# Performance work log

Measured on AMD Instinct MI355X. Metric: run time of the kernel, lower is better.

## Reference

```python
import jax, jax.numpy as jnp
import numpy as np

B, S, D, H = 4, 1024, 1024, 16
DH = D // H  # head_dim = 64


def setup_inputs() -> dict:
    key = jax.random.key(0)
    kq, kk, kv, kl, kwq, kwk, kwv, kwo = jax.random.split(key, 8)
    query = jax.random.normal(kq, (B, S, D), dtype=jnp.float32)
    key_t = jax.random.normal(kk, (B, S, D), dtype=jnp.float32)
    value = jax.random.normal(kv, (B, S, D), dtype=jnp.float32)
    # padding: keys at positions >= valid length are padded (True)
    lengths = jax.random.randint(kl, (B,), S // 2, S + 1)
    key_padding_mask = jnp.arange(S)[None, :] >= lengths[:, None]  # [B,S] bool
    scale = 1.0 / np.sqrt(D)
    Wq = jax.random.normal(kwq, (D, D), dtype=jnp.float32) * scale
    Wk = jax.random.normal(kwk, (D, D), dtype=jnp.float32) * scale
    Wv = jax.random.normal(kwv, (D, D), dtype=jnp.float32) * scale
    Wo = jax.random.normal(kwo, (D, D), dtype=jnp.float32) * scale
    gamma = jnp.ones((H,), dtype=jnp.float32)
    return {"query": query, "key": key_t, "value": value,
            "key_padding_mask": key_padding_mask,
            "Wq": Wq, "Wk": Wk, "Wv": Wv, "Wo": Wo, "gamma": gamma}


def reference(query, key, value, key_padding_mask, Wq, Wk, Wv, Wo, gamma):
    # nn.Linear(x) = x @ W.T (bias=False)
    q = jnp.einsum('bsd,ed->bse', query, Wq).reshape(B, S, H, DH).transpose(0, 2, 1, 3)  # [B,H,S,Dh]
    k = jnp.einsum('bsd,ed->bse', key, Wk).reshape(B, S, H, DH).transpose(0, 2, 1, 3)
    v = jnp.einsum('bsd,ed->bse', value, Wv).reshape(B, S, H, DH).transpose(0, 2, 1, 3)
    scores = jnp.einsum('bhqd,bhkd->bhqk', q, k) / jnp.sqrt(jnp.float32(DH))
    pad = key_padding_mask[:, None, None, :]  # [B,1,1,S]
    scores = jnp.where(pad, -jnp.inf, scores)
    v = jnp.where(key_padding_mask[:, None, :, None], 0.0, v)
    attn = jax.nn.softmax(scores, axis=-1)  # dropout p=0 (eval) -> identity
    ws = jnp.einsum('bhqk,bhkd->bhqd', attn, v)
    ws = ws * gamma[None, :, None, None]  # per-head scale
    ws = ws.transpose(0, 2, 1, 3).reshape(B, S, D)
    return jnp.einsum('bsd,ed->bse', ws, Wo)
```

## Files before the change

### kernel.cpp

```cpp
#include <hip/hip_runtime.h>
#include <math.h>

#define S_LEN 1024
#define DMODEL 1024

typedef __attribute__((ext_vector_type(8))) short bf16x8;
typedef __attribute__((ext_vector_type(4))) short bf16x4;
typedef __attribute__((ext_vector_type(4))) float f32x4;

#define MFMA16(a, b, c) __builtin_amdgcn_mfma_f32_16x16x32_bf16(a, b, c, 0, 0, 0)

#define WP (1024u * 1024u)
#define XP (4u * 1024u * 1024u)

__device__ __forceinline__ unsigned short rne_bf16(float f) {
    unsigned u = __float_as_uint(f);
    u += 0x7FFFu + ((u >> 16) & 1u);
    return (unsigned short)(u >> 16);
}

__device__ __forceinline__ void split_rne(float f, unsigned short& h, unsigned short& l) {
    unsigned short hh = rne_bf16(f);
    float lf = f - __uint_as_float(((unsigned)hh) << 16);
    h = hh;
    l = rne_bf16(lf);
}

typedef const __attribute__((address_space(1))) unsigned int* gas_t;
typedef __attribute__((address_space(3))) unsigned int* las_t;
__device__ __forceinline__ void glds16(const void* g, void* l) {
    __builtin_amdgcn_global_load_lds((gas_t)g, (las_t)l, 16, 0, 0);
}

__global__ __launch_bounds__(256)
void convert_wx(const float* __restrict__ W0, const float* __restrict__ W1,
                const float* __restrict__ W2, const float* __restrict__ W3,
                const float* __restrict__ Xq, const float* __restrict__ Xk,
                const float* __restrict__ Xv, const int* __restrict__ mask,
                unsigned short* __restrict__ Wpl, unsigned short* __restrict__ Xbase) {
    int blk = blockIdx.x;
    if (blk < 4096) {
        const int which = blk >> 10;
        const float* W = which == 0 ? W0 : which == 1 ? W1 : which == 2 ? W2 : W3;
        int i = ((blk & 1023) * 256 + threadIdx.x) * 4;
        float4 f = *(const float4*)&W[i];
        if (which == 3) {
            unsigned short* hi = Wpl + 3 * WP;
            unsigned short* lo = Wpl + 4 * WP;
            bf16x4 h, l;
            unsigned short hh, ll;
            split_rne(f.x, hh, ll); h[0] = (short)hh; l[0] = (short)ll;
            split_rne(f.y, hh, ll); h[1] = (short)hh; l[1] = (short)ll;
            split_rne(f.z, hh, ll); h[2] = (short)hh; l[2] = (short)ll;
            split_rne(f.w, hh, ll); h[3] = (short)hh; l[3] = (short)ll;
            *(bf16x4*)&hi[i] = h;
            *(bf16x4*)&lo[i] = l;
        } else {
            unsigned short* hi = Wpl + (size_t)which * WP;
            bf16x4 h;
            h[0] = (short)rne_bf16(f.x);
            h[1] = (short)rne_bf16(f.y);
            h[2] = (short)rne_bf16(f.z);
            h[3] = (short)rne_bf16(f.w);
            *(bf16x4*)&hi[i] = h;
        }
    } else {
        blk -= 4096;
        const int which = blk >> 12;
        const float* X = which == 0 ? Xq : which == 1 ? Xk : Xv;
        unsigned short* Xr = Xbase + (size_t)which * XP;
        int i = ((blk & 4095) * 256 + threadIdx.x) * 4;
        if (which != 0) {
            const int b = i >> 20, s = (i >> 10) & 1023;
            if (mask[b * 1024 + s]) {
                if (mask[b * 1024 + (s & ~127)]) return;
                bf16x4 zz = {0, 0, 0, 0};
                *(bf16x4*)&Xr[i] = zz;
                return;
            }
        }
        float4 f = *(const float4*)&X[i];
        bf16x4 h;
        h[0] = (short)rne_bf16(f.x);
        h[1] = (short)rne_bf16(f.y);
        h[2] = (short)rne_bf16(f.z);
        h[3] = (short)rne_bf16(f.w);
        *(bf16x4*)&Xr[i] = h;
    }
}

__global__ __launch_bounds__(256)
void gemm_proj(const unsigned short* __restrict__ Xbase,
               const unsigned short* __restrict__ Wpl,
               const int* __restrict__ mask,
               unsigned short* __restrict__ Obase) {
    __shared__ unsigned short AS[2][128 * 32];
    __shared__ unsigned short BS[2][128 * 32];

    const int z = blockIdx.z;
    const unsigned short* A = Xbase + (size_t)z * XP;
    const unsigned short* B = Wpl + (size_t)z * WP;

    const int t = threadIdx.x, lane = t & 63, w = t >> 6;
    const int quad = lane >> 4, l15 = lane & 15;
    const int wr = w & 1, wc = w >> 1;

    const int linb = blockIdx.x + (blockIdx.y << 3);
    const int swz = ((linb & 7) << 5) + (linb >> 3);
    const int bx = swz & 7, by = swz >> 3;
    const int rowBase = by * 128, colBase = bx * 128;

    if (z && mask[(by >> 3) * 1024 + ((by & 7) << 7)]) return;

    const unsigned short* gA[2];
    const unsigned short* gB[2];
    #pragma unroll
    for (int e = 0; e < 2; e++) {
        int row = w * 32 + e * 16 + (lane >> 2);
        int cg = (lane & 3) ^ ((row >> 1) & 3);
        gA[e] = A + (size_t)(rowBase + row) * 1024 + cg * 8;
        gB[e] = B + (size_t)(colBase + row) * 1024 + cg * 8;
    }
    const int ldA0 = (w * 32) * 32, ldA1 = (w * 32 + 16) * 32;

    int aAd[4], bAd[4];
    #pragma unroll
    for (int i = 0; i < 4; i++) {
        int ra = wr * 64 + i * 16 + l15;
        aAd[i] = ra * 32 + (quad ^ ((ra >> 1) & 3)) * 8;
        int rb = wc * 64 + i * 16 + l15;
        bAd[i] = rb * 32 + (quad ^ ((rb >> 1) & 3)) * 8;
    }

    f32x4 acc[4][4] = {};

    for (int kt = 0; kt < 16; kt++) {
        if (kt) __syncthreads();
        const int ko = kt * 64;
        glds16(gA[0] + ko,      &AS[0][ldA0]);
        glds16(gA[1] + ko,      &AS[0][ldA1]);
        glds16(gB[0] + ko,      &BS[0][ldA0]);
        glds16(gB[1] + ko,      &BS[0][ldA1]);
        glds16(gA[0] + ko + 32, &AS[1][ldA0]);
        glds16(gA[1] + ko + 32, &AS[1][ldA1]);
        glds16(gB[0] + ko + 32, &BS[1][ldA0]);
        glds16(gB[1] + ko + 32, &BS[1][ldA1]);
        __syncthreads();

        #pragma unroll
        for (int h2 = 0; h2 < 2; h2++) {
            bf16x8 af[4], bfr[4];
            #pragma unroll
            for (int i = 0; i < 4; i++) af[i] = *(const bf16x8*)&AS[h2][aAd[i]];
            #pragma unroll
            for (int j = 0; j < 4; j++) bfr[j] = *(const bf16x8*)&BS[h2][bAd[j]];
            #pragma unroll
            for (int j = 0; j < 4; j++)
                #pragma unroll
                for (int i = 0; i < 4; i++)
                    acc[i][j] = MFMA16(af[i], bfr[j], acc[i][j]);
        }
    }

    unsigned short* O = Obase + (size_t)z * XP;
    #pragma unroll
    for (int i = 0; i < 4; i++)
        #pragma unroll
        for (int j = 0; j < 4; j++) {
            const int m0 = rowBase + wr * 64 + i * 16 + quad * 4;
            const int n = colBase + wc * 64 + j * 16 + l15;
            const int bb = m0 >> 10, s = m0 & 1023, hh = n >> 6, dh = n & 63;
            const size_t hb = ((size_t)(bb * 16 + hh)) << 16;
            if (z == 2) {
                bf16x4 v4;
                #pragma unroll
                for (int r = 0; r < 4; r++) v4[r] = (short)rne_bf16(acc[i][j][r]);
                *(bf16x4*)&O[hb + (size_t)dh * 1024 + s] = v4;
            } else {
                #pragma unroll
                for (int r = 0; r < 4; r++)
                    O[hb + (size_t)(s + r) * 64 + dh] = rne_bf16(acc[i][j][r]);
            }
        }
}

__global__ __launch_bounds__(256)
void gemm_out2(const unsigned short* __restrict__ A,
               const unsigned short* __restrict__ Bh, const unsigned short* __restrict__ Bl,
               float* __restrict__ Cf) {
    __shared__ unsigned short AS[2][128 * 32];
    __shared__ unsigned short BhS[2][64 * 32], BlS[2][64 * 32];

    const int t = threadIdx.x, lane = t & 63, w = t >> 6;
    const int quad = lane >> 4, l15 = lane & 15;
    const int wr = w & 1, wc = w >> 1;

    const int linb = blockIdx.x + (blockIdx.y << 4);
    const int swz = ((linb & 7) << 6) + (linb >> 3);
    const int bx = swz & 15, by = swz >> 4;
    const int rowBase = by * 128, colBase = bx * 64;

    const unsigned short* gA[2];
    #pragma unroll
    for (int e = 0; e < 2; e++) {
        int row = w * 32 + e * 16 + (lane >> 2);
        int cg = (lane & 3) ^ ((row >> 1) & 3);
        gA[e] = A + (size_t)(rowBase + row) * 1024 + cg * 8;
    }
    const unsigned short *gBh, *gBl;
    {
        int row = w * 16 + (lane >> 2);
        int cg = (lane & 3) ^ ((row >> 1) & 3);
        gBh = Bh + (size_t)(colBase + row) * 1024 + cg * 8;
        gBl = Bl + (size_t)(colBase + row) * 1024 + cg * 8;
    }
    const int ldA0 = (w * 32) * 32, ldA1 = (w * 32 + 16) * 32;
    const int ldB = (w * 16) * 32;

    int aAd[4], bAd[2];
    #pragma unroll
    for (int i = 0; i < 4; i++) {
        int ra = wr * 64 + i * 16 + l15;
        aAd[i] = ra * 32 + (quad ^ ((ra >> 1) & 3)) * 8;
    }
    #pragma unroll
    for (int j = 0; j < 2; j++) {
        int rb = wc * 32 + j * 16 + l15;
        bAd[j] = rb * 32 + (quad ^ ((rb >> 1) & 3)) * 8;
    }

    f32x4 acc[4][2] = {};

    for (int kt = 0; kt < 16; kt++) {
        if (kt) __syncthreads();
        const int ko = kt * 64;
        glds16(gA[0] + ko,      &AS[0][ldA0]);
        glds16(gA[1] + ko,      &AS[0][ldA1]);
        glds16(gBh + ko,        &BhS[0][ldB]);
        glds16(gBl + ko,        &BlS[0][ldB]);
        glds16(gA[0] + ko + 32, &AS[1][ldA0]);
        glds16(gA[1] + ko + 32, &AS[1][ldA1]);
        glds16(gBh + ko + 32,   &BhS[1][ldB]);
        glds16(gBl + ko + 32,   &BlS[1][ldB]);
        __syncthreads();

        #pragma unroll
        for (int h2 = 0; h2 < 2; h2++) {
            bf16x8 af[4], bhf[2], blf[2];
            #pragma unroll
            for (int i = 0; i < 4; i++) af[i] = *(const bf16x8*)&AS[h2][aAd[i]];
            #pragma unroll
            for (int j = 0; j < 2; j++) {
                bhf[j] = *(const bf16x8*)&BhS[h2][bAd[j]];
                blf[j] = *(const bf16x8*)&BlS[h2][bAd[j]];
            }
            #pragma unroll
            for (int j = 0; j < 2; j++)
                #pragma unroll
                for (int i = 0; i < 4; i++) {
                    acc[i][j] = MFMA16(af[i], bhf[j], acc[i][j]);
                    acc[i][j] = MFMA16(af[i], blf[j], acc[i][j]);
                }
        }
    }

    #pragma unroll
    for (int i = 0; i < 4; i++)
        #pragma unroll
        for (int j = 0; j < 2; j++)
            #pragma unroll
            for (int r = 0; r < 4; r++) {
                int m = rowBase + wr * 64 + i * 16 + quad * 4 + r;
                int n = colBase + wc * 32 + j * 16 + l15;
                Cf[(size_t)m * 1024 + n] = acc[i][j][r];
            }
}

__global__ __launch_bounds__(256)
void attn_mfma(const unsigned short* __restrict__ Qr, const unsigned short* __restrict__ Kr,
               const unsigned short* __restrict__ Vt,
               const int* __restrict__ mask, const float* __restrict__ gamma,
               unsigned short* __restrict__ WSr) {
    __shared__ int maskS[1024];
    __shared__ unsigned short Ks[64 * 72];
    __shared__ unsigned short Vs[64 * 72];
    __shared__ unsigned short Ph[4 * 16 * 72];

    const int t = threadIdx.x, lane = t & 63, w = t >> 6;
    const int quad = lane >> 4, l15 = lane & 15;

    const int linb = blockIdx.x + (blockIdx.y << 4);
    const int swz = ((linb & 7) << 5) + (linb >> 3);
    const int qx = swz & 15, h = swz >> 4;

    const int q0 = qx * 64, b = blockIdx.z;
    const size_t hb = ((size_t)(b * 16 + h)) << 16;

    ((int4*)maskS)[t] = ((const int4*)(mask + b * 1024))[t];

    bf16x8 qhi[2];
    {
        const int qrow = q0 + w * 16 + l15;
        const size_t qb = hb + (size_t)qrow * 64 + quad * 8;
        qhi[0] = *(const bf16x8*)&Qr[qb];
        qhi[1] = *(const bf16x8*)&Qr[qb + 32];
    }

    const int sc = (t & 7) * 8;
    const int sr = t >> 3;

    f32x4 o[4] = {};
    float lsum[4] = {0.f, 0.f, 0.f, 0.f};

    bf16x8 kreg[2], vreg[2];
    #pragma unroll
    for (int e = 0; e < 2; e++) {
        int row = e * 32 + sr;
        kreg[e] = *(const bf16x8*)&Kr[hb + (size_t)row * 64 + sc];
        vreg[e] = *(const bf16x8*)&Vt[hb + (size_t)row * 1024 + sc];
    }
    __syncthreads();
    #pragma unroll
    for (int e = 0; e < 2; e++) {
        int row = e * 32 + sr;
        *(bf16x8*)&Ks[row * 72 + sc] = kreg[e];
        *(bf16x8*)&Vs[row * 72 + sc] = vreg[e];
    }
    __syncthreads();

    for (int jt = 0; jt < 16; jt++) {
        const int j0 = jt * 64;
        if (maskS[j0]) break;
        const bool partial = maskS[j0 + 63] != 0;
        const int j0n = j0 + 64;
        const bool pf = (jt < 15) && (maskS[j0n] == 0);

        if (pf) {
            #pragma unroll
            for (int e = 0; e < 2; e++) {
                int row = e * 32 + sr;
                kreg[e] = *(const bf16x8*)&Kr[hb + (size_t)(j0n + row) * 64 + sc];
                vreg[e] = *(const bf16x8*)&Vt[hb + (size_t)row * 1024 + j0n + sc];
            }
        }

        f32x4 s4[4] = {};
        __builtin_amdgcn_s_setprio(1);
        #pragma unroll
        for (int nj = 0; nj < 4; nj++) {
            int kr = (nj * 16 + l15) * 72 + quad * 8;
            #pragma unroll
            for (int kk = 0; kk < 2; kk++) {
                bf16x8 kv = *(const bf16x8*)&Ks[kr + kk * 32];
                s4[nj] = MFMA16(qhi[kk], kv, s4[nj]);
            }
        }
        __builtin_amdgcn_s_setprio(0);

        if (partial) {
            #pragma unroll
            for (int nj = 0; nj < 4; nj++) {
                int mk = maskS[j0 + nj * 16 + l15];
                #pragma unroll
                for (int r = 0; r < 4; r++) {
                    float p = mk ? 0.f : __expf(s4[nj][r] * 0.125f);
                    lsum[r] += p;
                    Ph[(w * 16 + quad * 4 + r) * 72 + nj * 16 + l15] = rne_bf16(p);
                }
            }
        } else {
            #pragma unroll
            for (int nj = 0; nj < 4; nj++) {
                #pragma unroll
                for (int r = 0; r < 4; r++) {
                    float p = __expf(s4[nj][r] * 0.125f);
                    lsum[r] += p;
                    Ph[(w * 16 + quad * 4 + r) * 72 + nj * 16 + l15] = rne_bf16(p);
                }
            }
        }

        bf16x8 ph[2];
        #pragma unroll
        for (int ks = 0; ks < 2; ks++)
            ph[ks] = *(const bf16x8*)&Ph[(w * 16 + l15) * 72 + ks * 32 + quad * 8];
        __builtin_amdgcn_s_setprio(1);
        #pragma unroll
        for (int dt = 0; dt < 4; dt++) {
            int vr = (dt * 16 + l15) * 72 + quad * 8;
            #pragma unroll
            for (int ks = 0; ks < 2; ks++) {
                bf16x8 vv = *(const bf16x8*)&Vs[vr + ks * 32];
                o[dt] = MFMA16(ph[ks], vv, o[dt]);
            }
        }
        __builtin_amdgcn_s_setprio(0);

        if (pf) {
            __syncthreads();
            #pragma unroll
            for (int e = 0; e < 2; e++) {
                int row = e * 32 + sr;
                *(bf16x8*)&Ks[row * 72 + sc] = kreg[e];
                *(bf16x8*)&Vs[row * 72 + sc] = vreg[e];
            }
            __syncthreads();
        }
    }

    #pragma unroll
    for (int r = 0; r < 4; r++) {
        lsum[r] += __shfl_xor(lsum[r], 1);
        lsum[r] += __shfl_xor(lsum[r], 2);
        lsum[r] += __shfl_xor(lsum[r], 4);
        lsum[r] += __shfl_xor(lsum[r], 8);
    }

    const float g = gamma[h];
    #pragma unroll
    for (int r = 0; r < 4; r++) {
        const int qrow = q0 + w * 16 + quad * 4 + r;
        const float sc2 = g / lsum[r];
        const size_t base = ((size_t)b * 1024 + qrow) * 1024 + h * 64;
        #pragma unroll
        for (int dt = 0; dt < 4; dt++)
            WSr[base + dt * 16 + l15] = rne_bf16(o[dt][r] * sc2);
    }
}

extern "C" void kernel_launch(void* const* d_in, const int* in_sizes, int n_in,
                              void* d_out, int out_size, void* d_ws, size_t ws_size,
                              hipStream_t stream) {
    const float* query = (const float*)d_in[0];
    const float* key   = (const float*)d_in[1];
    const float* value = (const float*)d_in[2];
    const int*   mask  = (const int*)d_in[3];
    const float* Wq    = (const float*)d_in[4];
    const float* Wk    = (const float*)d_in[5];
    const float* Wv    = (const float*)d_in[6];
    const float* Wo    = (const float*)d_in[7];
    const float* gamma = (const float*)d_in[8];
    float* out = (float*)d_out;

    unsigned short* u = (unsigned short*)d_ws;
    unsigned short* Xbase = u;
    unsigned short* Obase = u + 3 * XP;
    unsigned short* Wpl   = u + 6 * XP;
    unsigned short* WSr   = Xbase;
    unsigned short* Qr = Obase, *Kr = Obase + XP, *Vt = Obase + 2 * XP;
    unsigned short* Woh = Wpl + 3 * WP, *Wol = Wpl + 4 * WP;

    convert_wx<<<16384, 256, 0, stream>>>(Wq, Wk, Wv, Wo, query, key, value, mask, Wpl, Xbase);

    gemm_proj<<<dim3(8, 32, 3), 256, 0, stream>>>(Xbase, Wpl, mask, Obase);

    attn_mfma<<<dim3(16, 16, 4), 256, 0, stream>>>(Qr, Kr, Vt, mask, gamma, WSr);

    gemm_out2<<<dim3(16, 32), 256, 0, stream>>>(WSr, Woh, Wol, out);
}
```

Baseline: 197.8 us.

## Rewrite projection GEMM with 256x256 tiles and software-pipelined LDS prefetch

Restructures the QKV projection GEMM to use 512-thread blocks computing 256x256 output tiles with a 64-wide K step. The K-tile loads are double-buffered and interleaved with MFMA phases, using explicit ds_read asm, waitcnt and barriers, plus s_setprio around the MFMAs. The aim is to hide global-to-LDS latency and raise arithmetic intensity per block. In exchange it uses more LDS, gives fewer blocks (192 total, with masked blocks exiting early), and depends on fragile hand-managed synchronization.

```diff
diff --git a/kernel.cpp b/kernel.cpp
--- a/kernel.cpp
+++ b/kernel.cpp
@@ -30,6 +30,12 @@
 typedef __attribute__((address_space(3))) unsigned int* las_t;
 __device__ __forceinline__ void glds16(const void* g, void* l) {
     __builtin_amdgcn_global_load_lds((gas_t)g, (las_t)l, 16, 0, 0);
+}
+
+__device__ __forceinline__ bf16x8 dsr(unsigned a) {
+    bf16x8 r;
+    asm volatile("ds_read_b128 %0, %1" : "=v"(r) : "v"(a));
+    return r;
 }
 
 __global__ __launch_bounds__(256)
@@ -89,86 +95,139 @@
     }
 }
 
-__global__ __launch_bounds__(256)
+__global__ __launch_bounds__(512, 1)
 void gemm_proj(const unsigned short* __restrict__ Xbase,
                const unsigned short* __restrict__ Wpl,
                const int* __restrict__ mask,
                unsigned short* __restrict__ Obase) {
-    __shared__ unsigned short AS[2][128 * 32];
-    __shared__ unsigned short BS[2][128 * 32];
-
-    const int z = blockIdx.z;
+    __shared__ unsigned short As[2][2][128 * 64];
+    __shared__ unsigned short Bs[2][2][128 * 64];
+
+    const int t = threadIdx.x, lane = t & 63, w = t >> 6;
+    const int quad = lane >> 4, l15 = lane & 15;
+    const int wm = w >> 2, wn = w & 3;
+
+    const int g = blockIdx.z * 64 + blockIdx.y * 4 + blockIdx.x;
+    const int sg = (g & 7) * 24 + (g >> 3);
+    const int z = sg >> 6, rem = sg & 63;
+    const int rowBase = (rem >> 2) * 256, colBase = (rem & 3) * 256;
+
+    if (z && mask[(rowBase >> 10) * 1024 + (rowBase & 1023)]) return;
+
     const unsigned short* A = Xbase + (size_t)z * XP;
     const unsigned short* B = Wpl + (size_t)z * WP;
 
-    const int t = threadIdx.x, lane = t & 63, w = t >> 6;
-    const int quad = lane >> 4, l15 = lane & 15;
-    const int wr = w & 1, wc = w >> 1;
-
-    const int linb = blockIdx.x + (blockIdx.y << 3);
-    const int swz = ((linb & 7) << 5) + (linb >> 3);
-    const int bx = swz & 7, by = swz >> 3;
-    const int rowBase = by * 128, colBase = bx * 128;
-
-    if (z && mask[(by >> 3) * 1024 + ((by & 7) << 7)]) return;
-
-    const unsigned short* gA[2];
-    const unsigned short* gB[2];
-    #pragma unroll
-    for (int e = 0; e < 2; e++) {
-        int row = w * 32 + e * 16 + (lane >> 2);
-        int cg = (lane & 3) ^ ((row >> 1) & 3);
-        gA[e] = A + (size_t)(rowBase + row) * 1024 + cg * 8;
-        gB[e] = B + (size_t)(colBase + row) * 1024 + cg * 8;
-    }
-    const int ldA0 = (w * 32) * 32, ldA1 = (w * 32 + 16) * 32;
-
-    int aAd[4], bAd[4];
-    #pragma unroll
-    for (int i = 0; i < 4; i++) {
-        int ra = wr * 64 + i * 16 + l15;
-        aAd[i] = ra * 32 + (quad ^ ((ra >> 1) & 3)) * 8;
-        int rb = wc * 64 + i * 16 + l15;
-        bAd[i] = rb * 32 + (quad ^ ((rb >> 1) & 3)) * 8;
-    }
-
-    f32x4 acc[4][4] = {};
+    const unsigned short* gAs[2][2];
+    const unsigned short* gBs[2][2];
+    #pragma unroll
+    for (int h = 0; h < 2; h++)
+        #pragma unroll
+        for (int r = 0; r < 2; r++) {
+            int lrow = r * 64 + w * 8 + (lane >> 3);
+            int cg = (lane & 7) ^ (lrow & 7);
+            gAs[h][r] = A + (size_t)(rowBase + h * 128 + lrow) * 1024 + cg * 8;
+            gBs[h][r] = B + (size_t)(colBase + h * 128 + lrow) * 1024 + cg * 8;
+        }
+    const int ld0 = (w * 8) * 64, ld1 = (64 + w * 8) * 64;
+
+    const unsigned asB = (unsigned)(size_t)&As[0][0][0];
+    const unsigned bsB = (unsigned)(size_t)&Bs[0][0][0];
+    unsigned aAd[8][2], bAd[4][2];
+    #pragma unroll
+    for (int i = 0; i < 8; i++)
+        #pragma unroll
+        for (int kk = 0; kk < 2; kk++) {
+            int lr = i * 16 + l15;
+            aAd[i][kk] = asB + wm * 16384 + lr * 128 + ((((kk << 2) + quad) ^ (lr & 7)) << 4);
+        }
+    #pragma unroll
+    for (int j = 0; j < 4; j++)
+        #pragma unroll
+        for (int kk = 0; kk < 2; kk++) {
+            int lr = (wn & 1) * 64 + j * 16 + l15;
+            bAd[j][kk] = bsB + (wn >> 1) * 16384 + lr * 128 + ((((kk << 2) + quad) ^ (lr & 7)) << 4);
+        }
+
+    f32x4 acc[8][4] = {};
+
+    glds16(gAs[0][0], &As[0][0][ld0]);
+    glds16(gAs[0][1], &As[0][0][ld1]);
+    glds16(gAs[1][0], &As[0][1][ld0]);
+    glds16(gAs[1][1], &As[0][1][ld1]);
+    glds16(gBs[0][0], &Bs[0][0][ld0]);
+    glds16(gBs[0][1], &Bs[0][0][ld1]);
+    glds16(gBs[1][0], &Bs[0][1][ld0]);
+    glds16(gBs[1][1], &Bs[0][1][ld1]);
+    glds16(gBs[0][0] + 64, &Bs[1][0][ld0]);
+    glds16(gBs[0][1] + 64, &Bs[1][0][ld1]);
+    glds16(gBs[1][0] + 64, &Bs[1][1][ld0]);
+    glds16(gBs[1][1] + 64, &Bs[1][1][ld1]);
+    asm volatile("s_waitcnt vmcnt(4)");
+    __builtin_amdgcn_sched_barrier(0);
+    __builtin_amdgcn_s_barrier();
 
     for (int kt = 0; kt < 16; kt++) {
-        if (kt) __syncthreads();
-        const int ko = kt * 64;
-        glds16(gA[0] + ko,      &AS[0][ldA0]);
-        glds16(gA[1] + ko,      &AS[0][ldA1]);
-        glds16(gB[0] + ko,      &BS[0][ldA0]);
-        glds16(gB[1] + ko,      &BS[0][ldA1]);
-        glds16(gA[0] + ko + 32, &AS[1][ldA0]);
-        glds16(gA[1] + ko + 32, &AS[1][ldA1]);
-        glds16(gB[0] + ko + 32, &BS[1][ldA0]);
-        glds16(gB[1] + ko + 32, &BS[1][ldA1]);
-        __syncthreads();
-
-        #pragma unroll
-        for (int h2 = 0; h2 < 2; h2++) {
-            bf16x8 af[4], bfr[4];
-            #pragma unroll
-            for (int i = 0; i < 4; i++) af[i] = *(const bf16x8*)&AS[h2][aAd[i]];
-            #pragma unroll
-            for (int j = 0; j < 4; j++) bfr[j] = *(const bf16x8*)&BS[h2][bAd[j]];
-            #pragma unroll
-            for (int j = 0; j < 4; j++)
-                #pragma unroll
-                for (int i = 0; i < 4; i++)
-                    acc[i][j] = MFMA16(af[i], bfr[j], acc[i][j]);
+        const int buf = kt & 1;
+        const unsigned bo = buf * 32768;
+        bf16x8 bfr[4][2];
+        #pragma unroll
+        for (int p = 0; p < 4; p++) {
+            bf16x8 af[2][2];
+            af[0][0] = dsr(aAd[2 * p + 0][0] + bo);
+            af[0][1] = dsr(aAd[2 * p + 0][1] + bo);
+            af[1][0] = dsr(aAd[2 * p + 1][0] + bo);
+            af[1][1] = dsr(aAd[2 * p + 1][1] + bo);
+            if (p == 0) {
+                #pragma unroll
+                for (int j = 0; j < 4; j++) {
+                    bfr[j][0] = dsr(bAd[j][0] + bo);
+                    bfr[j][1] = dsr(bAd[j][1] + bo);
+                }
+            }
+            if (p == 0 && kt + 1 < 16) {
+                glds16(gAs[0][0] + (kt + 1) * 64, &As[buf ^ 1][0][ld0]);
+                glds16(gAs[0][1] + (kt + 1) * 64, &As[buf ^ 1][0][ld1]);
+            }
+            if (p == 1 && kt + 1 < 16) {
+                glds16(gAs[1][0] + (kt + 1) * 64, &As[buf ^ 1][1][ld0]);
+                glds16(gAs[1][1] + (kt + 1) * 64, &As[buf ^ 1][1][ld1]);
+            }
+            if (p == 2 && kt + 2 < 16) {
+                glds16(gBs[0][0] + (kt + 2) * 64, &Bs[buf][0][ld0]);
+                glds16(gBs[0][1] + (kt + 2) * 64, &Bs[buf][0][ld1]);
+            }
+            if (p == 3 && kt + 2 < 16) {
+                glds16(gBs[1][0] + (kt + 2) * 64, &Bs[buf][1][ld0]);
+                glds16(gBs[1][1] + (kt + 2) * 64, &Bs[buf][1][ld1]);
+            }
+            __builtin_amdgcn_s_barrier();
+            asm volatile("s_waitcnt lgkmcnt(0)");
+            __builtin_amdgcn_sched_barrier(0);
+            __builtin_amdgcn_s_setprio(1);
+            #pragma unroll
+            for (int ii = 0; ii < 2; ii++)
+                #pragma unroll
+                for (int j = 0; j < 4; j++)
+                    #pragma unroll
+                    for (int kk = 0; kk < 2; kk++)
+                        acc[2 * p + ii][j] = MFMA16(af[ii][kk], bfr[j][kk], acc[2 * p + ii][j]);
+            __builtin_amdgcn_s_setprio(0);
+            if (p == 3) {
+                if (kt < 14) asm volatile("s_waitcnt vmcnt(4)");
+                else         asm volatile("s_waitcnt vmcnt(0)");
+                __builtin_amdgcn_sched_barrier(0);
+            }
+            __builtin_amdgcn_s_barrier();
         }
     }
 
     unsigned short* O = Obase + (size_t)z * XP;
     #pragma unroll
-    for (int i = 0; i < 4; i++)
+    for (int i = 0; i < 8; i++)
         #pragma unroll
         for (int j = 0; j < 4; j++) {
-            const int m0 = rowBase + wr * 64 + i * 16 + quad * 4;
-            const int n = colBase + wc * 64 + j * 16 + l15;
+            const int m0 = rowBase + wm * 128 + i * 16 + quad * 4;
+            const int n = colBase + wn * 64 + j * 16 + l15;
             const int bb = m0 >> 10, s = m0 & 1023, hh = n >> 6, dh = n & 63;
             const size_t hb = ((size_t)(bb * 16 + hh)) << 16;
             if (z == 2) {
@@ -452,7 +511,7 @@
 
     convert_wx<<<16384, 256, 0, stream>>>(Wq, Wk, Wv, Wo, query, key, value, mask, Wpl, Xbase);
 
-    gemm_proj<<<dim3(8, 32, 3), 256, 0, stream>>>(Xbase, Wpl, mask, Obase);
+    gemm_proj<<<dim3(4, 16, 3), 512, 0, stream>>>(Xbase, Wpl, mask, Obase);
 
     attn_mfma<<<dim3(16, 16, 4), 256, 0, stream>>>(Qr, Kr, Vt, mask, gamma, WSr);
 
```

Result: slower. 201.9 us (+2.1%).
